# Optimization experiments

Measured on AMD Instinct MI355X. Metric: run time of the kernel, lower is better.

## Reference

```python
import jax, jax.numpy as jnp
import numpy as np

OUT_F, IN_F, RANK = 3072, 3072, 64
B, S = 2, 4096


def setup_inputs() -> dict:
    key = jax.random.key(0)
    k_x, k_w, k_s, k_a, k_b, k_bias = jax.random.split(key, 6)
    x = jax.random.normal(k_x, (B, S, IN_F), dtype=jnp.float32)
    # ternary weights in {-1, 0, +1}
    weight_q = jax.random.randint(k_w, (OUT_F, IN_F), 0, 3, dtype=jnp.int32) - 1
    # per-output-channel absmean scale, strictly positive
    scale = jax.random.uniform(k_s, (OUT_F, 1), dtype=jnp.float32) * 0.05 + 1e-3
    lora_A = jax.random.normal(k_a, (OUT_F, RANK), dtype=jnp.float32) * 0.01
    lora_B = jax.random.normal(k_b, (RANK, IN_F), dtype=jnp.float32) * 0.01
    bias = jax.random.normal(k_bias, (OUT_F,), dtype=jnp.float32)
    return {"x": x, "weight_q": weight_q, "scale": scale,
            "lora_A": lora_A, "lora_B": lora_B, "bias": bias}


def reference(x, weight_q, scale, lora_A, lora_B, bias):
    # W_q cast up to activation dtype (dequant), dense matmul: [b,s,in] @ [in,out]
    Wq = weight_q.astype(x.dtype)
    out = jnp.einsum('bsi,oi->bso', x, Wq) * scale.reshape(1, 1, -1)
    # LoRA low-rank residual: x @ B^T @ A^T
    out = out + jnp.einsum('bsr,or->bso', jnp.einsum('bsi,ri->bsr', x, lora_B), lora_A)
    out = out + bias
    return out
```

## Files before the change

kernel.cpp:

```cpp
#include <hip/hip_runtime.h>
#include <hip/hip_bf16.h>

#define M_DIM 8192
#define N_DIM 3072
#define K_DIM 3072
#define RANK_ 64

#define BM 256
#define BN 192
#define BK 64
#define NT (K_DIM / BK)

typedef __attribute__((ext_vector_type(8))) __bf16 bf16x8;
typedef __attribute__((ext_vector_type(4))) float floatx4;
typedef __attribute__((ext_vector_type(8))) unsigned short ushort8;

__device__ __forceinline__ unsigned short f2bf(float f) {
  union { float f; unsigned u; } v;
  v.f = f;
  return (unsigned short)((v.u + 0x7fffu + ((v.u >> 16) & 1u)) >> 16);
}

__global__ void cvt_x_kernel(const float* __restrict__ x, unsigned short* __restrict__ xb) {
  size_t i = ((size_t)blockIdx.x * 256u + threadIdx.x) * 8u;
  const float4* xp = (const float4*)(x + i);
  float4 a = xp[0];
  float4 b = xp[1];
  ushort8 r;
  r[0] = f2bf(a.x); r[1] = f2bf(a.y); r[2] = f2bf(a.z); r[3] = f2bf(a.w);
  r[4] = f2bf(b.x); r[5] = f2bf(b.y); r[6] = f2bf(b.z); r[7] = f2bf(b.w);
  *(ushort8*)(xb + i) = r;
}

__global__ __launch_bounds__(256) void build_weff_kernel(
    const int* __restrict__ wq, const float* __restrict__ scale,
    const float* __restrict__ lA, const float* __restrict__ lB,
    unsigned short* __restrict__ weff) {
  __shared__ float sB[64][128];
  __shared__ float sA[128][65];

  const int tid = threadIdx.x;
  const int i0 = blockIdx.x * 128;
  const int o0 = blockIdx.y * 128;

#pragma unroll
  for (int l = 0; l < 8; ++l) {
    int lin = l * 256 + tid;
    int r = lin >> 5;
    int c4 = (lin & 31) * 4;
    *(float4*)&sB[r][c4] = *(const float4*)&lB[(size_t)r * K_DIM + i0 + c4];
  }
#pragma unroll
  for (int l = 0; l < 8; ++l) {
    int lin = l * 256 + tid;
    int o = lin >> 4;
    int c4 = (lin & 15) * 4;
    *(float4*)&sA[o][c4] = *(const float4*)&lA[(size_t)(o0 + o) * RANK_ + c4];
  }
  __syncthreads();

  const int ib = (tid & 15) * 8;
  const int ob = (tid >> 4) * 8;

  float acc[8][8];
#pragma unroll
  for (int oo = 0; oo < 8; ++oo) {
    const int o = o0 + ob + oo;
    const float sc = scale[o];
    const int* wrow = wq + (size_t)o * K_DIM + i0 + ib;
    int4 w0 = *(const int4*)wrow;
    int4 w1 = *(const int4*)(wrow + 4);
    acc[oo][0] = (float)w0.x * sc; acc[oo][1] = (float)w0.y * sc;
    acc[oo][2] = (float)w0.z * sc; acc[oo][3] = (float)w0.w * sc;
    acc[oo][4] = (float)w1.x * sc; acc[oo][5] = (float)w1.y * sc;
    acc[oo][6] = (float)w1.z * sc; acc[oo][7] = (float)w1.w * sc;
  }

  for (int r = 0; r < RANK_; ++r) {
    float4 b0 = *(const float4*)&sB[r][ib];
    float4 b1 = *(const float4*)&sB[r][ib + 4];
#pragma unroll
    for (int oo = 0; oo < 8; ++oo) {
      const float a = sA[ob + oo][r];
      acc[oo][0] += a * b0.x; acc[oo][1] += a * b0.y;
      acc[oo][2] += a * b0.z; acc[oo][3] += a * b0.w;
      acc[oo][4] += a * b1.x; acc[oo][5] += a * b1.y;
      acc[oo][6] += a * b1.z; acc[oo][7] += a * b1.w;
    }
  }

#pragma unroll
  for (int oo = 0; oo < 8; ++oo) {
    ushort8 pk;
#pragma unroll
    for (int ii = 0; ii < 8; ++ii) pk[ii] = f2bf(acc[oo][ii]);
    *(ushort8*)&weff[(size_t)(o0 + ob + oo) * K_DIM + i0 + ib] = pk;
  }
}

#define MF(A,B,C) __builtin_amdgcn_mfma_f32_16x16x32_bf16(A, B, C, 0, 0, 0)
#define MFMA12(MB) do { \
  acc[MB+0][0]=MF(a0,b0,acc[MB+0][0]); acc[MB+0][1]=MF(a0,b1,acc[MB+0][1]); acc[MB+0][2]=MF(a0,b2,acc[MB+0][2]); \
  acc[MB+1][0]=MF(a1,b0,acc[MB+1][0]); acc[MB+1][1]=MF(a1,b1,acc[MB+1][1]); acc[MB+1][2]=MF(a1,b2,acc[MB+1][2]); \
  acc[MB+2][0]=MF(a2,b0,acc[MB+2][0]); acc[MB+2][1]=MF(a2,b1,acc[MB+2][1]); acc[MB+2][2]=MF(a2,b2,acc[MB+2][2]); \
  acc[MB+3][0]=MF(a3,b0,acc[MB+3][0]); acc[MB+3][1]=MF(a3,b1,acc[MB+3][1]); acc[MB+3][2]=MF(a3,b2,acc[MB+3][2]); \
} while (0)

#define ABASE(b) ((b) * 16384)
#define BBASE(b) (32768 + (b) * 12288)

__global__ __launch_bounds__(512, 2) void gemm8_kernel(
    const unsigned short* __restrict__ xb, const unsigned short* __restrict__ weff,
    const float* __restrict__ bias, float* __restrict__ out) {
  extern __shared__ unsigned short smem[];

  const int tid = threadIdx.x;
  const int lane = tid & 63;
  const int wid = tid >> 6;
  const int wm = wid >> 2;
  const int wn = wid & 3;

  const int bid = blockIdx.x;
  const int swz = (bid & 7) * 64 + (bid >> 3);
  const int tileM = swz / (N_DIM / BN);
  const int tileN = swz % (N_DIM / BN);
  const int rowA0 = tileM * BM;
  const int colB0 = tileN * BN;

  const int srow = tid >> 3;
  const int skidx = ((tid & 7) * 8) ^ ((srow & 7) << 3);
  const unsigned short* gAbase = xb + (size_t)(rowA0 + srow) * K_DIM + skidx;
  const unsigned short* gBbase = weff + (size_t)(colB0 + srow) * K_DIM + skidx;
  const int ldsLin = tid * 8;

  auto stageA2 = [&](int t, int h) {
    const int b = t & 1;
    const unsigned short* g = gAbase + (size_t)t * BK;
#pragma unroll
    for (int l = h * 2; l < h * 2 + 2; ++l)
      __builtin_amdgcn_global_load_lds(
          (const __attribute__((address_space(1))) void*)(g + (size_t)l * 64 * K_DIM),
          (__attribute__((address_space(3))) void*)&smem[ABASE(b) + l * 4096 + ldsLin], 16, 0, 0);
  };
  auto stageB = [&](int t) {
    const int b = t & 1;
    const unsigned short* g = gBbase + (size_t)t * BK;
#pragma unroll
    for (int l = 0; l < 3; ++l)
      __builtin_amdgcn_global_load_lds(
          (const __attribute__((address_space(1))) void*)(g + (size_t)l * 64 * K_DIM),
          (__attribute__((address_space(3))) void*)&smem[BBASE(b) + l * 4096 + ldsLin], 16, 0, 0);
  };

  const int lrow = lane & 15;
  const int khalf = lane >> 4;
  const int rsw = (lrow & 7) << 3;
  auto ldA = [&](int b, int mf, int kk) -> bf16x8 {
    return *(const bf16x8*)&smem[ABASE(b) + (wm * 128 + mf * 16 + lrow) * 64 +
                                 ((kk * 32 + khalf * 8) ^ rsw)];
  };
  auto ldB = [&](int b, int nf, int kk) -> bf16x8 {
    return *(const bf16x8*)&smem[BBASE(b) + (wn * 48 + nf * 16 + lrow) * 64 +
                                 ((kk * 32 + khalf * 8) ^ rsw)];
  };

  floatx4 acc[8][3];
#pragma unroll
  for (int m = 0; m < 8; ++m)
#pragma unroll
    for (int n = 0; n < 3; ++n)
      acc[m][n] = (floatx4){0.f, 0.f, 0.f, 0.f};

  stageB(0); stageA2(0, 0); stageA2(0, 1); stageB(1);
  asm volatile("s_waitcnt vmcnt(3)" ::: "memory");
  __builtin_amdgcn_s_barrier();

  bf16x8 a0, a1, a2, a3, b0, b1, b2;
#pragma unroll 2
  for (int g = 0; g < NT; ++g) {
    const int bf = g & 1;
    a0 = ldA(bf, 0, 0); a1 = ldA(bf, 1, 0); a2 = ldA(bf, 2, 0); a3 = ldA(bf, 3, 0);
    b0 = ldB(bf, 0, 0); b1 = ldB(bf, 1, 0); b2 = ldB(bf, 2, 0);
    if (g + 1 < NT) stageA2(g + 1, 0);
    __builtin_amdgcn_s_barrier();
    asm volatile("s_waitcnt lgkmcnt(0)" ::: "memory");
    __builtin_amdgcn_s_setprio(1);
    MFMA12(0);
    __builtin_amdgcn_s_setprio(0);
    __builtin_amdgcn_s_barrier();
    a0 = ldA(bf, 4, 0); a1 = ldA(bf, 5, 0); a2 = ldA(bf, 6, 0); a3 = ldA(bf, 7, 0);
    if (g + 1 < NT) stageA2(g + 1, 1);
    __builtin_amdgcn_s_barrier();
    asm volatile("s_waitcnt lgkmcnt(0)" ::: "memory");
    __builtin_amdgcn_s_setprio(1);
    MFMA12(4);
    __builtin_amdgcn_s_setprio(0);
    __builtin_amdgcn_s_barrier();
    a0 = ldA(bf, 0, 1); a1 = ldA(bf, 1, 1); a2 = ldA(bf, 2, 1); a3 = ldA(bf, 3, 1);
    b0 = ldB(bf, 0, 1); b1 = ldB(bf, 1, 1); b2 = ldB(bf, 2, 1);
    __builtin_amdgcn_s_barrier();
    asm volatile("s_waitcnt lgkmcnt(0)" ::: "memory");
    __builtin_amdgcn_s_setprio(1);
    MFMA12(0);
    __builtin_amdgcn_s_setprio(0);
    __builtin_amdgcn_s_barrier();
    a0 = ldA(bf, 4, 1); a1 = ldA(bf, 5, 1); a2 = ldA(bf, 6, 1); a3 = ldA(bf, 7, 1);
    if (g + 2 < NT) stageB(g + 2);
    __builtin_amdgcn_s_barrier();
    asm volatile("s_waitcnt lgkmcnt(0)" ::: "memory");
    __builtin_amdgcn_s_setprio(1);
    MFMA12(4);
    __builtin_amdgcn_s_setprio(0);
    if (g < NT - 2) asm volatile("s_waitcnt vmcnt(3)" ::: "memory");
    else            asm volatile("s_waitcnt vmcnt(0)" ::: "memory");
    __builtin_amdgcn_s_barrier();
  }

  const int orow0 = rowA0 + wm * 128;
  const int ocol0 = colB0 + wn * 48;
#pragma unroll
  for (int nf = 0; nf < 3; ++nf) {
    const int col = ocol0 + nf * 16 + lrow;
    const float bvs = bias[col];
#pragma unroll
    for (int mf = 0; mf < 8; ++mf) {
      const int r0 = orow0 + mf * 16 + khalf * 4;
#pragma unroll
      for (int j = 0; j < 4; ++j)
        out[(size_t)(r0 + j) * N_DIM + col] = acc[mf][nf][j] + bvs;
    }
  }
}

extern "C" void kernel_launch(void* const* d_in, const int* in_sizes, int n_in,
                              void* d_out, int out_size, void* d_ws, size_t ws_size,
                              hipStream_t stream) {
  const float* x = (const float*)d_in[0];
  const int* wq = (const int*)d_in[1];
  const float* scale = (const float*)d_in[2];
  const float* lA = (const float*)d_in[3];
  const float* lB = (const float*)d_in[4];
  const float* bias = (const float*)d_in[5];
  float* out = (float*)d_out;

  unsigned short* xb = (unsigned short*)d_ws;
  unsigned short* weff = xb + (size_t)M_DIM * K_DIM;

  hipFuncSetAttribute((const void*)gemm8_kernel,
                      hipFuncAttributeMaxDynamicSharedMemorySize, 114688);

  cvt_x_kernel<<<(M_DIM * (size_t)K_DIM) / (8 * 256), 256, 0, stream>>>(x, xb);
  build_weff_kernel<<<dim3(K_DIM / 128, N_DIM / 128), 256, 0, stream>>>(wq, scale, lA, lB, weff);
  gemm8_kernel<<<(M_DIM / BM) * (N_DIM / BN), 512, 114688, stream>>>(xb, weff, bias, out);
}
```

Measured before the change: 354.7 us.

## Triple-buffer B tiles and halve sync phases in the bf16 MFMA main loop

The GEMM main loop goes from four load/compute phases per K-tile to two. Each phase loads all eight A fragments and three B fragments, then issues 24 MFMAs, so there are fewer barriers and longer uninterrupted MFMA runs. The B tile is now triple-buffered (g%3) and A is staged with a single 4-load call into a double buffer. Dynamic LDS grows to 139264 bytes. This costs more fragment registers and LDS, and may limit occupancy.

```diff
diff --git a/kernel.cpp b/kernel.cpp
--- a/kernel.cpp
+++ b/kernel.cpp
@@ -99,12 +99,6 @@
 }
 
 #define MF(A,B,C) __builtin_amdgcn_mfma_f32_16x16x32_bf16(A, B, C, 0, 0, 0)
-#define MFMA12(MB) do { \
-  acc[MB+0][0]=MF(a0,b0,acc[MB+0][0]); acc[MB+0][1]=MF(a0,b1,acc[MB+0][1]); acc[MB+0][2]=MF(a0,b2,acc[MB+0][2]); \
-  acc[MB+1][0]=MF(a1,b0,acc[MB+1][0]); acc[MB+1][1]=MF(a1,b1,acc[MB+1][1]); acc[MB+1][2]=MF(a1,b2,acc[MB+1][2]); \
-  acc[MB+2][0]=MF(a2,b0,acc[MB+2][0]); acc[MB+2][1]=MF(a2,b1,acc[MB+2][1]); acc[MB+2][2]=MF(a2,b2,acc[MB+2][2]); \
-  acc[MB+3][0]=MF(a3,b0,acc[MB+3][0]); acc[MB+3][1]=MF(a3,b1,acc[MB+3][1]); acc[MB+3][2]=MF(a3,b2,acc[MB+3][2]); \
-} while (0)
 
 #define ABASE(b) ((b) * 16384)
 #define BBASE(b) (32768 + (b) * 12288)
@@ -133,23 +127,21 @@
   const unsigned short* gBbase = weff + (size_t)(colB0 + srow) * K_DIM + skidx;
   const int ldsLin = tid * 8;
 
-  auto stageA2 = [&](int t, int h) {
-    const int b = t & 1;
+  auto stageA = [&](int t, int buf) {
     const unsigned short* g = gAbase + (size_t)t * BK;
 #pragma unroll
-    for (int l = h * 2; l < h * 2 + 2; ++l)
+    for (int l = 0; l < 4; ++l)
       __builtin_amdgcn_global_load_lds(
           (const __attribute__((address_space(1))) void*)(g + (size_t)l * 64 * K_DIM),
-          (__attribute__((address_space(3))) void*)&smem[ABASE(b) + l * 4096 + ldsLin], 16, 0, 0);
-  };
-  auto stageB = [&](int t) {
-    const int b = t & 1;
+          (__attribute__((address_space(3))) void*)&smem[ABASE(buf) + l * 4096 + ldsLin], 16, 0, 0);
+  };
+  auto stageB = [&](int t, int buf) {
     const unsigned short* g = gBbase + (size_t)t * BK;
 #pragma unroll
     for (int l = 0; l < 3; ++l)
       __builtin_amdgcn_global_load_lds(
           (const __attribute__((address_space(1))) void*)(g + (size_t)l * 64 * K_DIM),
-          (__attribute__((address_space(3))) void*)&smem[BBASE(b) + l * 4096 + ldsLin], 16, 0, 0);
+          (__attribute__((address_space(3))) void*)&smem[BBASE(buf) + l * 4096 + ldsLin], 16, 0, 0);
   };
 
   const int lrow = lane & 15;
@@ -171,45 +163,41 @@
     for (int n = 0; n < 3; ++n)
       acc[m][n] = (floatx4){0.f, 0.f, 0.f, 0.f};
 
-  stageB(0); stageA2(0, 0); stageA2(0, 1); stageB(1);
+  stageB(0, 0); stageA(0, 0); stageB(1, 1);
   asm volatile("s_waitcnt vmcnt(3)" ::: "memory");
   __builtin_amdgcn_s_barrier();
 
-  bf16x8 a0, a1, a2, a3, b0, b1, b2;
-#pragma unroll 2
+  bf16x8 a[8], b[3];
+#pragma unroll 6
   for (int g = 0; g < NT; ++g) {
-    const int bf = g & 1;
-    a0 = ldA(bf, 0, 0); a1 = ldA(bf, 1, 0); a2 = ldA(bf, 2, 0); a3 = ldA(bf, 3, 0);
-    b0 = ldB(bf, 0, 0); b1 = ldB(bf, 1, 0); b2 = ldB(bf, 2, 0);
-    if (g + 1 < NT) stageA2(g + 1, 0);
+    const int bfA = g & 1;
+    const int bfB = g % 3;
+#pragma unroll
+    for (int m = 0; m < 8; ++m) a[m] = ldA(bfA, m, 0);
+#pragma unroll
+    for (int n = 0; n < 3; ++n) b[n] = ldB(bfB, n, 0);
+    if (g + 1 < NT) stageA(g + 1, (g + 1) & 1);
     __builtin_amdgcn_s_barrier();
     asm volatile("s_waitcnt lgkmcnt(0)" ::: "memory");
     __builtin_amdgcn_s_setprio(1);
-    MFMA12(0);
+#pragma unroll
+    for (int m = 0; m < 8; ++m)
+#pragma unroll
+      for (int n = 0; n < 3; ++n) acc[m][n] = MF(a[m], b[n], acc[m][n]);
     __builtin_amdgcn_s_setprio(0);
     __builtin_amdgcn_s_barrier();
-    a0 = ldA(bf, 4, 0); a1 = ldA(bf, 5, 0); a2 = ldA(bf, 6, 0); a3 = ldA(bf, 7, 0);
-    if (g + 1 < NT) stageA2(g + 1, 1);
+#pragma unroll
+    for (int m = 0; m < 8; ++m) a[m] = ldA(bfA, m, 1);
+#pragma unroll
+    for (int n = 0; n < 3; ++n) b[n] = ldB(bfB, n, 1);
+    if (g + 2 < NT) stageB(g + 2, (g + 2) % 3);
     __builtin_amdgcn_s_barrier();
     asm volatile("s_waitcnt lgkmcnt(0)" ::: "memory");
     __builtin_amdgcn_s_setprio(1);
-    MFMA12(4);
-    __builtin_amdgcn_s_setprio(0);
-    __builtin_amdgcn_s_barrier();
-    a0 = ldA(bf, 0, 1); a1 = ldA(bf, 1, 1); a2 = ldA(bf, 2, 1); a3 = ldA(bf, 3, 1);
-    b0 = ldB(bf, 0, 1); b1 = ldB(bf, 1, 1); b2 = ldB(bf, 2, 1);
-    __builtin_amdgcn_s_barrier();
-    asm volatile("s_waitcnt lgkmcnt(0)" ::: "memory");
-    __builtin_amdgcn_s_setprio(1);
-    MFMA12(0);
-    __builtin_amdgcn_s_setprio(0);
-    __builtin_amdgcn_s_barrier();
-    a0 = ldA(bf, 4, 1); a1 = ldA(bf, 5, 1); a2 = ldA(bf, 6, 1); a3 = ldA(bf, 7, 1);
-    if (g + 2 < NT) stageB(g + 2);
-    __builtin_amdgcn_s_barrier();
-    asm volatile("s_waitcnt lgkmcnt(0)" ::: "memory");
-    __builtin_amdgcn_s_setprio(1);
-    MFMA12(4);
+#pragma unroll
+    for (int m = 0; m < 8; ++m)
+#pragma unroll
+      for (int n = 0; n < 3; ++n) acc[m][n] = MF(a[m], b[n], acc[m][n]);
     __builtin_amdgcn_s_setprio(0);
     if (g < NT - 2) asm volatile("s_waitcnt vmcnt(3)" ::: "memory");
     else            asm volatile("s_waitcnt vmcnt(0)" ::: "memory");
@@ -247,9 +235,9 @@
   unsigned short* weff = xb + (size_t)M_DIM * K_DIM;
 
   hipFuncSetAttribute((const void*)gemm8_kernel,
-                      hipFuncAttributeMaxDynamicSharedMemorySize, 114688);
+                      hipFuncAttributeMaxDynamicSharedMemorySize, 139264);
 
   cvt_x_kernel<<<(M_DIM * (size_t)K_DIM) / (8 * 256), 256, 0, stream>>>(x, xb);
   build_weff_kernel<<<dim3(K_DIM / 128, N_DIM / 128), 256, 0, stream>>>(wq, scale, lA, lB, weff);
-  gemm8_kernel<<<(M_DIM / BM) * (N_DIM / BN), 512, 114688, stream>>>(xb, weff, bias, out);
-}
+  gemm8_kernel<<<(M_DIM / BM) * (N_DIM / BN), 512, 139264, stream>>>(xb, weff, bias, out);
+}
```

After: 356.6 us. About the same (+0.5%).
